# Kernel tuning notes

Measured on AMD Instinct MI355X. Metric: run time of the kernel, lower is better.

The kernel has to match this reference:

```python
import jax, jax.numpy as jnp
import numpy as np

SMOOTH = 1.0
MAX_DIST = 10


def _neighbor_conv(x):
    # 3x3 ones kernel with zero center, padding=1 (NCHW, C=1)
    k = jnp.ones((1, 1, 3, 3), x.dtype).at[0, 0, 1, 1].set(0.0)
    return jax.lax.conv_general_dilated(
        x, k, window_strides=(1, 1), padding=[(1, 1), (1, 1)],
        dimension_numbers=('NCHW', 'OIHW', 'NCHW'))


def _analyze_skeleton(skel):
    n = _neighbor_conv(skel)
    on = skel > 0.5
    endpoints = ((n == 1) & on).astype(skel.dtype)
    midpoints = ((n == 2) & on).astype(skel.dtype)
    junctions = ((n > 2) & on).astype(skel.dtype)
    return endpoints, midpoints, junctions


def _iou(p, g):
    inter = jnp.sum(p * g, axis=(2, 3))
    union = jnp.sum(p, axis=(2, 3)) + jnp.sum(g, axis=(2, 3)) - inter
    return (inter + SMOOTH) / (union + SMOOTH)


def _structural_similarity(pred_skel, gt_skel):
    pe, pm, pj = _analyze_skeleton(pred_skel)
    ge, gm, gj = _analyze_skeleton(gt_skel)
    e_iou, m_iou, j_iou = _iou(pe, ge), _iou(pm, gm), _iou(pj, gj)
    ge_c = jnp.sum(ge, axis=(2, 3))
    gj_c = jnp.sum(gj, axis=(2, 3))
    gm_c = jnp.sum(gm, axis=(2, 3))
    total = ge_c + gj_c + gm_c + SMOOTH
    loss = 1.0 - ((ge_c / total) * e_iou + (gj_c / total) * j_iou + (gm_c / total) * m_iou)
    return loss.mean()


def _maxpool3(x):
    return jax.lax.reduce_window(
        x, -jnp.inf, jax.lax.max,
        window_dimensions=(1, 1, 3, 3), window_strides=(1, 1, 1, 1),
        padding=[(0, 0), (0, 0), (1, 1), (1, 1)])


def _distance_approximation(target, reference):
    # Fixed MAX_DIST iterations; identical math to the torch early-exit loop
    # because new_points requires ~found_mask (no distance is overwritten).
    tgt_on = target > 0.5

    def step(carry, d):
        dilated, found, dist = carry
        dilated = _maxpool3(dilated)
        new = (dilated > 0.5) & tgt_on & (~found)
        dist = dist + d.astype(dist.dtype) * new.astype(dist.dtype)
        return (dilated, found | new, dist), None

    init = (reference, jnp.zeros(target.shape, bool), jnp.zeros_like(target))
    (_, found, dist), _ = jax.lax.scan(step, init, jnp.arange(1, MAX_DIST + 1, dtype=jnp.int32))
    unfound = tgt_on & (~found)
    dist = dist + jnp.asarray(MAX_DIST, dist.dtype) * unfound.astype(dist.dtype)
    total_points = jnp.sum(tgt_on.astype(dist.dtype), axis=(2, 3))
    return jnp.sum(dist, axis=(2, 3)) / (total_points + SMOOTH)


def _medial_axis_distance(pred_skel, gt_skel):
    p2g = _distance_approximation(pred_skel, gt_skel)
    g2p = _distance_approximation(gt_skel, pred_skel)
    return (((p2g + g2p) / 2.0) / MAX_DIST).mean()


def setup_inputs() -> dict:
    key = jax.random.key(0)
    k1, k2 = jax.random.split(key)
    B, C, H, W = 32, 1, 512, 512
    pred_skel = jax.random.uniform(k1, (B, C, H, W), dtype=jnp.float32)
    gt_skel = (jax.random.uniform(k2, (B, C, H, W), dtype=jnp.float32) < 0.1).astype(jnp.float32)
    return {"pred_skel": pred_skel, "gt_skel": gt_skel}


def reference(pred_skel, gt_skel):
    inter = jnp.sum(pred_skel * gt_skel, axis=(2, 3))
    psum = jnp.sum(pred_skel, axis=(2, 3))
    gsum = jnp.sum(gt_skel, axis=(2, 3))
    dice = (2.0 * inter + SMOOTH) / (psum + gsum + SMOOTH)
    dice_loss = 1.0 - dice.mean()
    structural_loss = _structural_similarity(pred_skel, gt_skel)
    medial_loss = _medial_axis_distance(pred_skel, gt_skel)
    avg_mag = (dice_loss + structural_loss + medial_loss) / 3.0
    bal_dice = dice_loss / (dice_loss + SMOOTH) * avg_mag
    bal_struct = structural_loss / (structural_loss + SMOOTH) * avg_mag
    bal_medial = medial_loss / (medial_loss + SMOOTH) * avg_mag
    return bal_dice + bal_struct + bal_medial
```

## Files before the change

kernel.cpp:

```cpp
#include <hip/hip_runtime.h>
#include <stdint.h>

#define BATCH 32
#define H 512
#define W 512
#define NACC 16
#define TH 32
#define HALO 9
#define RH (TH + 2*HALO)
#define NWORDS (RH*8)
#define NT 1024
#define NW (NT/64)
#define NTILE (H/TH)
#define NBLK (NTILE*BATCH)


__global__ __launch_bounds__(NT, 4) void fused_kernel(
    const float* __restrict__ pred, const float* __restrict__ gt,
    float* __restrict__ part)
{
    __shared__ uint64_t MpS[NWORDS + 2];
    __shared__ uint64_t MgS[NWORDS + 2];
    __shared__ float    EC[2][TH];
    __shared__ float    redf[NW][2];
    __shared__ unsigned redu[NW][5];

    uint64_t* Mp = MpS + 1;
    uint64_t* Mg = MgS + 1;

    int fid  = blockIdx.x;
    int b    = fid & 31;
    int tile = fid >> 5;

    const float* pimg = pred + (size_t)b * H * W;
    const float* gimg = gt   + (size_t)b * H * W;
    int y0 = tile * TH;
    int tid = threadIdx.x, lane = tid & 63, wid = tid >> 6;

    float v0 = 0.f, v1 = 0.f;
    for (int s0 = wid; s0 < NWORDS; s0 += 4 * NW) {
        float vp[4], vg[4];
        #pragma unroll
        for (int u = 0; u < 4; ++u) {
            int s = s0 + u * NW;
            vp[u] = 0.f; vg[u] = 0.f;
            int ry = y0 - HALO + (s >> 3);
            if (s < NWORDS && (unsigned)ry < (unsigned)H) {
                int i0 = ry * W + (s & 7) * 64 + lane;
                vp[u] = pimg[i0]; vg[u] = gimg[i0];
            }
        }
        #pragma unroll
        for (int u = 0; u < 4; ++u) {
            int s = s0 + u * NW;
            if (s < NWORDS) {
                unsigned long long mp = __ballot(vp[u] > 0.5f);
                unsigned long long mg = __ballot(vg[u] > 0.5f);
                if (lane == 0) { Mp[s] = mp; Mg[s] = mg; }
                int r = s >> 3;
                if (r >= HALO && r < HALO + TH) {
                    v1 += vp[u];
                    v0 += (vg[u] > 0.5f) ? vp[u] : 0.f;
                }
            }
        }
    }
    if (tid == 0) { MpS[0] = 0; MpS[NWORDS + 1] = 0; MgS[0] = 0; MgS[NWORDS + 1] = 0; }

    bool isStencil = tid >= 512;
    int idx = tid & 511;
    int qi = idx & 127, h2 = idx >> 7;
    int x4 = qi * 4;
    int ys = y0 + h2 * 8;
    float4 pm4 = make_float4(0, 0, 0, 0), pc4 = make_float4(0, 0, 0, 0);
    if (isStencil) {
        if (ys > 0) pm4 = *(const float4*)(pimg + (size_t)(ys - 1) * W + x4);
        pc4 = *(const float4*)(pimg + (size_t)ys * W + x4);
    }

    if (tid < 2 * TH) {
        int c = tid >> 5, r = tid & (TH - 1);
        int y = y0 + r, col = 255 + c;
        float sum = (y > 0     ? pimg[(size_t)(y - 1) * W + col] : 0.f)
                  +              pimg[(size_t)y * W + col]
                  + (y < H - 1 ? pimg[(size_t)(y + 1) * W + col] : 0.f);
        EC[c][r] = sum;
    }
    __syncthreads();

    uint64_t cpack = 0ULL;
    int dsum = 0, dcnt = 0;

    if (isStencil) {
        int wdx = qi >> 4;
        int ss = (qi & 15) * 4;
        auto win6 = [&](int rb) -> uint32_t {
            const uint64_t* row = &Mg[rb * 8];
            uint64_t bm = row[wdx];
            if (ss == 0) {
                uint64_t lo = wdx ? row[wdx - 1] : 0ULL;
                return (uint32_t)(((bm << 1) | (lo >> 63)) & 0x3FULL);
            }
            uint32_t v = (uint32_t)((bm >> (ss - 1)) & 0x3FULL);
            if (ss == 60) {
                uint64_t hi = (wdx < 7) ? row[wdx + 1] : 0ULL;
                v |= ((uint32_t)hi & 1u) << 5;
            }
            return v;
        };
        int rb0 = h2 * 8 + HALO - 1;
        uint32_t wU = win6(rb0), wM = win6(rb0 + 1);

        for (int r = 0; r < 8; ++r) {
            int y = ys + r;
            float4 pp4 = (y < H - 1) ? *(const float4*)(pimg + (size_t)(y + 1) * W + x4)
                                     : make_float4(0, 0, 0, 0);
            uint32_t wD = win6(rb0 + 2 + r);
            int ry = h2 * 8 + r;

            float ps[6];
            ps[1] = pm4.x + pc4.x + pp4.x; ps[2] = pm4.y + pc4.y + pp4.y;
            ps[3] = pm4.z + pc4.z + pp4.z; ps[4] = pm4.w + pc4.w + pp4.w;
            float psl = __shfl_up(ps[4], 1, 64);
            float psr = __shfl_down(ps[1], 1, 64);
            if (lane == 0)  psl = (qi == 0)   ? 0.f : EC[0][ry];
            if (lane == 63) psr = (qi == 127) ? 0.f : EC[1][ry];
            ps[0] = psl; ps[5] = psr;

            float pcv[4] = {pc4.x, pc4.y, pc4.z, pc4.w};
            #pragma unroll
            for (int j = 0; j < 4; ++j) {
                float np = ps[j] + ps[j + 1] + ps[j + 2] - pcv[j];
                bool pon = pcv[j] > 0.5f;
                bool pe  = pon && (np == 1.f);
                bool pmb = pon && (np == 2.f);
                bool pjb = pon && (np > 2.f);
                uint32_t n9 = ((wU >> j) & 7u) | (((wM >> j) & 7u) << 3) | (((wD >> j) & 7u) << 6);
                uint32_t cen = (wM >> (j + 1)) & 1u;
                int ng = __popc(n9) - (int)cen;
                bool gon = cen != 0u;
                bool ge  = gon && (ng == 1);
                bool gmb = gon && (ng == 2);
                bool gjb = gon && (ng > 2);
                cpack += (uint64_t)pe
                       | ((uint64_t)pmb << 7)
                       | ((uint64_t)pjb << 14)
                       | ((uint64_t)ge  << 21)
                       | ((uint64_t)gmb << 28)
                       | ((uint64_t)gjb << 35)
                       | ((uint64_t)(pe  && ge)  << 42)
                       | ((uint64_t)(pmb && gmb) << 49)
                       | ((uint64_t)(pjb && gjb) << 56);
            }
            pm4 = pc4; pc4 = pp4; wU = wM; wM = wD;
        }
    } else {
        bool isP = tid < 256;
        int di = tid & 255;
        int o  = (HALO + (di >> 3)) * 8 + (di & 7);
        int w  = di & 7;
        bool wL = (w > 0), wR = (w < 7);
        const uint64_t* MT = isP ? Mp : Mg;
        const uint64_t* MV = isP ? Mg : Mp;

        uint64_t T = MT[o];
        dcnt = __popcll(T);
        dsum = dcnt;
        uint64_t VM = MV[o];
        uint64_t VL = wL ? MV[o - 1] : 0ULL;
        uint64_t VR = wR ? MV[o + 1] : 0ULL;
        uint64_t C = VM;

        #pragma unroll
        for (int a = 1; a <= 9; ++a) {
            int lo = o - 8 * a, hi = o + 8 * a;
            uint64_t NM = MV[lo] | MV[hi];
            uint64_t NL = wL ? (MV[lo - 1] | MV[hi - 1]) : 0ULL;
            uint64_t NR = wR ? (MV[lo + 1] | MV[hi + 1]) : 0ULL;
            uint64_t SL = NL, SM = NM, SR = NR;
            const int m = a - 1;
            if (m >= 1) {
                SM |= (SM << 1) | (SM >> 1) | (SL >> 63) | (SR << 63);
                SL |= SL << 1; SR |= SR >> 1;
            }
            if (m >= 2) {
                const int s = (m == 2) ? 1 : 2;
                SM |= (SM << s) | (SM >> s) | (SL >> (64 - s)) | (SR << (64 - s));
                SL |= SL << s; SR |= SR >> s;
            }
            if (m >= 4) {
                const int s = (m - 3 < 4) ? (m - 3) : 4;
                SM |= (SM << s) | (SM >> s) | (SL >> (64 - s)) | (SR << (64 - s));
                SL |= SL << s; SR |= SR >> s;
            }
            if (m >= 8) {
                const int s = m - 7;
                SM |= (SM << s) | (SM >> s) | (SL >> (64 - s)) | (SR << (64 - s));
                SL |= SL << s; SR |= SR >> s;
            }
            C |= SM;
            VL |= NL; VM |= NM; VR |= NR;
            C |= (VM << a) | (VM >> a) | (VL >> (64 - a)) | (VR << (64 - a));
            dsum += __popcll(T & ~C);
        }
    }

    unsigned r0, r1, r2, r3, r4;
    if (isStencil) {
        unsigned c3  = (unsigned)( cpack        & 0x7F);
        unsigned c4  = (unsigned)((cpack >> 7 ) & 0x7F);
        unsigned c5  = (unsigned)((cpack >> 14) & 0x7F);
        unsigned c6  = (unsigned)((cpack >> 21) & 0x7F);
        unsigned c7  = (unsigned)((cpack >> 28) & 0x7F);
        unsigned c8  = (unsigned)((cpack >> 35) & 0x7F);
        unsigned c9  = (unsigned)((cpack >> 42) & 0x7F);
        unsigned c10 = (unsigned)((cpack >> 49) & 0x7F);
        unsigned c11 = (unsigned)((cpack >> 56) & 0x7F);
        r0 = c3 | (c4 << 16); r1 = c5 | (c6 << 16); r2 = c7 | (c8 << 16);
        r3 = c9 | (c10 << 16); r4 = c11;
    } else {
        r0 = (unsigned)dsum | ((unsigned)dcnt << 16);
        r1 = 0; r2 = 0; r3 = 0; r4 = 0;
    }
    #pragma unroll
    for (int off = 32; off; off >>= 1) {
        v0 += __shfl_down(v0, off, 64);
        v1 += __shfl_down(v1, off, 64);
        r0 += __shfl_down(r0, off, 64);
        r1 += __shfl_down(r1, off, 64);
        r2 += __shfl_down(r2, off, 64);
        r3 += __shfl_down(r3, off, 64);
        r4 += __shfl_down(r4, off, 64);
    }
    if (lane == 0) {
        redf[wid][0] = v0; redf[wid][1] = v1;
        redu[wid][0] = r0; redu[wid][1] = r1; redu[wid][2] = r2;
        redu[wid][3] = r3; redu[wid][4] = r4;
    }
    __syncthreads();
    if (tid < 16) {
        int k = tid;
        float s = 0.f;
        if (k < 2) {
            #pragma unroll
            for (int wv = 0; wv < NW; ++wv) s += redf[wv][k];
        } else if (k == 2) {
            unsigned u = 0;
            for (int wv = 4; wv < 8; ++wv) u += redu[wv][0] >> 16;
            s = (float)u;
        } else if (k <= 10) {
            int pair = (k - 3) >> 1, hi = (k - 3) & 1;
            unsigned u = 0;
            for (int wv = 8; wv < 16; ++wv) u += (redu[wv][pair] >> (hi * 16)) & 0xFFFFu;
            s = (float)u;
        } else if (k == 11) {
            unsigned u = 0;
            for (int wv = 8; wv < 16; ++wv) u += redu[wv][4];
            s = (float)u;
        } else {
            int base = (k < 14) ? 0 : 4, hi = k & 1;
            unsigned u = 0;
            for (int wv = base; wv < base + 4; ++wv)
                u += (redu[wv][0] >> (hi * 16)) & 0xFFFFu;
            s = (float)u;
        }
        part[fid * NACC + k] = s;
    }
}

__global__ __launch_bounds__(512) void final_kernel(
    const float* __restrict__ part, float* __restrict__ out)
{
    __shared__ float sacc[BATCH][NACC];
    __shared__ float tri[BATCH][3];
    int t = threadIdx.x;
    {
        int b = t >> 4, k = t & 15;
        float s = 0.f;
        #pragma unroll 4
        for (int j = 0; j < NTILE; ++j)
            s += part[((j << 5) + b) * NACC + k];
        sacc[b][k] = s;
    }
    __syncthreads();
    if (t < BATCH) {
        const float* a = sacc[t];
        float inter = a[0], psum = a[1], gsum = a[2];
        float dice = (2.f * inter + 1.f) / (psum + gsum + 1.f);

        float pe = a[3], pm = a[4], pj = a[5];
        float ge = a[6], gm = a[7], gj = a[8];
        float ie = a[9], im = a[10], ij = a[11];
        float e_iou = (ie + 1.f) / (pe + ge - ie + 1.f);
        float m_iou = (im + 1.f) / (pm + gm - im + 1.f);
        float j_iou = (ij + 1.f) / (pj + gj - ij + 1.f);
        float total = ge + gj + gm + 1.f;
        float sloss = 1.f - ((ge / total) * e_iou + (gj / total) * j_iou + (gm / total) * m_iou);

        float p2g = a[12] / (a[13] + 1.f);
        float g2p = a[14] / (a[15] + 1.f);
        float med = ((p2g + g2p) * 0.5f) / 10.f;
        tri[t][0] = dice; tri[t][1] = sloss; tri[t][2] = med;
    }
    __syncthreads();
    if (t == 0) {
        float dice = 0.f, sloss = 0.f, med = 0.f;
        for (int b = 0; b < BATCH; ++b) {
            dice += tri[b][0]; sloss += tri[b][1]; med += tri[b][2];
        }
        float dice_loss  = 1.f - dice / (float)BATCH;
        float structural = sloss / (float)BATCH;
        float medial     = med / (float)BATCH;
        float avg = (dice_loss + structural + medial) / 3.f;
        float r = dice_loss  / (dice_loss  + 1.f) * avg
                + structural / (structural + 1.f) * avg
                + medial     / (medial     + 1.f) * avg;
        out[0] = r;
    }
}

extern "C" void kernel_launch(void* const* d_in, const int* in_sizes, int n_in,
                              void* d_out, int out_size, void* d_ws, size_t ws_size,
                              hipStream_t stream)
{
    const float* pred = (const float*)d_in[0];
    const float* gt   = (const float*)d_in[1];
    float* part = (float*)d_ws;
    float* out  = (float*)d_out;

    fused_kernel<<<dim3(NBLK), NT, 0, stream>>>(pred, gt, part);
    final_kernel<<<1, 512, 0, stream>>>(part, out);
}
```

Before: 117.7 us.

## Rebalance stencil rows between stencil and distance thread groups

The stencil work (8 rows per band) is split so the stencil half of the block handles 6 rows per band, and the distance-transform half also processes 2 rows per band after finishing its dilation work. This evens out load between the two thread halves, which previously had unequal work and left one half idle at the barrier. The reduction gains a sixth accumulator slot so distance counts and stencil counts from all warps can be summed separately. This adds register pressure and code size in the distance path.

```diff
diff --git a/kernel.cpp b/kernel.cpp
--- a/kernel.cpp
+++ b/kernel.cpp
@@ -23,7 +23,7 @@
     __shared__ uint64_t MgS[NWORDS + 2];
     __shared__ float    EC[2][TH];
     __shared__ float    redf[NW][2];
-    __shared__ unsigned redu[NW][5];
+    __shared__ unsigned redu[NW][6];
 
     uint64_t* Mp = MpS + 1;
     uint64_t* Mg = MgS + 1;
@@ -68,14 +68,16 @@
     if (tid == 0) { MpS[0] = 0; MpS[NWORDS + 1] = 0; MgS[0] = 0; MgS[NWORDS + 1] = 0; }
 
     bool isStencil = tid >= 512;
-    int idx = tid & 511;
-    int qi = idx & 127, h2 = idx >> 7;
+    int sidx = tid & 511;
+    int qi = sidx & 127, band = sidx >> 7;
+    int ysS = y0 + band * 6;
+    int ysD = y0 + 24 + band * 2;
+
     int x4 = qi * 4;
-    int ys = y0 + h2 * 8;
     float4 pm4 = make_float4(0, 0, 0, 0), pc4 = make_float4(0, 0, 0, 0);
     if (isStencil) {
-        if (ys > 0) pm4 = *(const float4*)(pimg + (size_t)(ys - 1) * W + x4);
-        pc4 = *(const float4*)(pimg + (size_t)ys * W + x4);
+        if (ysS > 0) pm4 = *(const float4*)(pimg + (size_t)(ysS - 1) * W + x4);
+        pc4 = *(const float4*)(pimg + (size_t)ysS * W + x4);
     }
 
     if (tid < 2 * TH) {
@@ -91,43 +93,42 @@
     uint64_t cpack = 0ULL;
     int dsum = 0, dcnt = 0;
 
-    if (isStencil) {
-        int wdx = qi >> 4;
-        int ss = (qi & 15) * 4;
-        auto win6 = [&](int rb) -> uint32_t {
-            const uint64_t* row = &Mg[rb * 8];
-            uint64_t bm = row[wdx];
-            if (ss == 0) {
-                uint64_t lo = wdx ? row[wdx - 1] : 0ULL;
-                return (uint32_t)(((bm << 1) | (lo >> 63)) & 0x3FULL);
-            }
-            uint32_t v = (uint32_t)((bm >> (ss - 1)) & 0x3FULL);
-            if (ss == 60) {
-                uint64_t hi = (wdx < 7) ? row[wdx + 1] : 0ULL;
-                v |= ((uint32_t)hi & 1u) << 5;
-            }
-            return v;
-        };
-        int rb0 = h2 * 8 + HALO - 1;
+    int wdx = qi >> 4;
+    int ss = (qi & 15) * 4;
+    auto win6 = [&](int rb) -> uint32_t {
+        const uint64_t* row = &Mg[rb * 8];
+        uint64_t bm = row[wdx];
+        if (ss == 0) {
+            uint64_t lo = wdx ? row[wdx - 1] : 0ULL;
+            return (uint32_t)(((bm << 1) | (lo >> 63)) & 0x3FULL);
+        }
+        uint32_t v = (uint32_t)((bm >> (ss - 1)) & 0x3FULL);
+        if (ss == 60) {
+            uint64_t hi = (wdx < 7) ? row[wdx + 1] : 0ULL;
+            v |= ((uint32_t)hi & 1u) << 5;
+        }
+        return v;
+    };
+    auto do_stencil = [&](int ys, int nrows, float4 m4, float4 c4) {
+        int rb0 = (ys - y0) + HALO - 1;
         uint32_t wU = win6(rb0), wM = win6(rb0 + 1);
-
-        for (int r = 0; r < 8; ++r) {
+        for (int r = 0; r < nrows; ++r) {
             int y = ys + r;
             float4 pp4 = (y < H - 1) ? *(const float4*)(pimg + (size_t)(y + 1) * W + x4)
                                      : make_float4(0, 0, 0, 0);
             uint32_t wD = win6(rb0 + 2 + r);
-            int ry = h2 * 8 + r;
+            int ry = (ys - y0) + r;
 
             float ps[6];
-            ps[1] = pm4.x + pc4.x + pp4.x; ps[2] = pm4.y + pc4.y + pp4.y;
-            ps[3] = pm4.z + pc4.z + pp4.z; ps[4] = pm4.w + pc4.w + pp4.w;
+            ps[1] = m4.x + c4.x + pp4.x; ps[2] = m4.y + c4.y + pp4.y;
+            ps[3] = m4.z + c4.z + pp4.z; ps[4] = m4.w + c4.w + pp4.w;
             float psl = __shfl_up(ps[4], 1, 64);
             float psr = __shfl_down(ps[1], 1, 64);
             if (lane == 0)  psl = (qi == 0)   ? 0.f : EC[0][ry];
             if (lane == 63) psr = (qi == 127) ? 0.f : EC[1][ry];
             ps[0] = psl; ps[5] = psr;
 
-            float pcv[4] = {pc4.x, pc4.y, pc4.z, pc4.w};
+            float pcv[4] = {c4.x, c4.y, c4.z, c4.w};
             #pragma unroll
             for (int j = 0; j < 4; ++j) {
                 float np = ps[j] + ps[j + 1] + ps[j + 2] - pcv[j];
@@ -152,8 +153,12 @@
                        | ((uint64_t)(pmb && gmb) << 49)
                        | ((uint64_t)(pjb && gjb) << 56);
             }
-            pm4 = pc4; pc4 = pp4; wU = wM; wM = wD;
-        }
+            m4 = c4; c4 = pp4; wU = wM; wM = wD;
+        }
+    };
+
+    if (isStencil) {
+        do_stencil(ysS, 6, pm4, pc4);
     } else {
         bool isP = tid < 256;
         int di = tid & 255;
@@ -203,25 +208,27 @@
             C |= (VM << a) | (VM >> a) | (VL >> (64 - a)) | (VR << (64 - a));
             dsum += __popcll(T & ~C);
         }
-    }
-
-    unsigned r0, r1, r2, r3, r4;
-    if (isStencil) {
-        unsigned c3  = (unsigned)( cpack        & 0x7F);
-        unsigned c4  = (unsigned)((cpack >> 7 ) & 0x7F);
-        unsigned c5  = (unsigned)((cpack >> 14) & 0x7F);
-        unsigned c6  = (unsigned)((cpack >> 21) & 0x7F);
-        unsigned c7  = (unsigned)((cpack >> 28) & 0x7F);
-        unsigned c8  = (unsigned)((cpack >> 35) & 0x7F);
-        unsigned c9  = (unsigned)((cpack >> 42) & 0x7F);
-        unsigned c10 = (unsigned)((cpack >> 49) & 0x7F);
-        unsigned c11 = (unsigned)((cpack >> 56) & 0x7F);
-        r0 = c3 | (c4 << 16); r1 = c5 | (c6 << 16); r2 = c7 | (c8 << 16);
-        r3 = c9 | (c10 << 16); r4 = c11;
-    } else {
-        r0 = (unsigned)dsum | ((unsigned)dcnt << 16);
-        r1 = 0; r2 = 0; r3 = 0; r4 = 0;
-    }
+        float4 m4 = make_float4(0, 0, 0, 0);
+        if (ysD > 0) m4 = *(const float4*)(pimg + (size_t)(ysD - 1) * W + x4);
+        float4 c4 = *(const float4*)(pimg + (size_t)ysD * W + x4);
+        do_stencil(ysD, 2, m4, c4);
+    }
+
+    unsigned c3  = (unsigned)( cpack        & 0x7F);
+    unsigned c4v = (unsigned)((cpack >> 7 ) & 0x7F);
+    unsigned c5  = (unsigned)((cpack >> 14) & 0x7F);
+    unsigned c6  = (unsigned)((cpack >> 21) & 0x7F);
+    unsigned c7  = (unsigned)((cpack >> 28) & 0x7F);
+    unsigned c8  = (unsigned)((cpack >> 35) & 0x7F);
+    unsigned c9  = (unsigned)((cpack >> 42) & 0x7F);
+    unsigned c10 = (unsigned)((cpack >> 49) & 0x7F);
+    unsigned c11 = (unsigned)((cpack >> 56) & 0x7F);
+    unsigned r0 = c3 | (c4v << 16);
+    unsigned r1 = c5 | (c6 << 16);
+    unsigned r2 = c7 | (c8 << 16);
+    unsigned r3 = c9 | (c10 << 16);
+    unsigned r4 = c11;
+    unsigned r5 = isStencil ? 0u : ((unsigned)dsum | ((unsigned)dcnt << 16));
     #pragma unroll
     for (int off = 32; off; off >>= 1) {
         v0 += __shfl_down(v0, off, 64);
@@ -231,11 +238,12 @@
         r2 += __shfl_down(r2, off, 64);
         r3 += __shfl_down(r3, off, 64);
         r4 += __shfl_down(r4, off, 64);
+        r5 += __shfl_down(r5, off, 64);
     }
     if (lane == 0) {
         redf[wid][0] = v0; redf[wid][1] = v1;
         redu[wid][0] = r0; redu[wid][1] = r1; redu[wid][2] = r2;
-        redu[wid][3] = r3; redu[wid][4] = r4;
+        redu[wid][3] = r3; redu[wid][4] = r4; redu[wid][5] = r5;
     }
     __syncthreads();
     if (tid < 16) {
@@ -246,22 +254,22 @@
             for (int wv = 0; wv < NW; ++wv) s += redf[wv][k];
         } else if (k == 2) {
             unsigned u = 0;
-            for (int wv = 4; wv < 8; ++wv) u += redu[wv][0] >> 16;
+            for (int wv = 4; wv < 8; ++wv) u += redu[wv][5] >> 16;
             s = (float)u;
         } else if (k <= 10) {
             int pair = (k - 3) >> 1, hi = (k - 3) & 1;
             unsigned u = 0;
-            for (int wv = 8; wv < 16; ++wv) u += (redu[wv][pair] >> (hi * 16)) & 0xFFFFu;
+            for (int wv = 0; wv < NW; ++wv) u += (redu[wv][pair] >> (hi * 16)) & 0xFFFFu;
             s = (float)u;
         } else if (k == 11) {
             unsigned u = 0;
-            for (int wv = 8; wv < 16; ++wv) u += redu[wv][4];
+            for (int wv = 0; wv < NW; ++wv) u += redu[wv][4];
             s = (float)u;
         } else {
             int base = (k < 14) ? 0 : 4, hi = k & 1;
             unsigned u = 0;
             for (int wv = base; wv < base + 4; ++wv)
-                u += (redu[wv][0] >> (hi * 16)) & 0xFFFFu;
+                u += (redu[wv][5] >> (hi * 16)) & 0xFFFFu;
             s = (float)u;
         }
         part[fid * NACC + k] = s;
```

After: 122.2 us. 1.04x slower.
